# Kernel optimization log

Measured on AMD Instinct MI355X. Metric: run time of the kernel, lower is better.

## Reference

```python
import jax, jax.numpy as jnp
import numpy as np

B, S, D, H, E, K = 2, 2048, 1024, 16, 8, 2
HD = D // H          # head dim = 64 (single shared KV head: MQA)
HID = 4 * D          # MoE expert hidden dim


def _rmsnorm(x):
    # zeta SimpleRMSNorm: F.normalize(x, dim=-1) * dim**0.5
    n = jnp.linalg.norm(x, axis=-1, keepdims=True)
    return x / jnp.maximum(n, 1e-12) * (D ** 0.5)


def setup_inputs() -> dict:
    key = jax.random.key(0)
    ks = jax.random.split(key, 8)
    def w(k, shape, fan_in):
        return jax.random.normal(k, shape, jnp.float32) * (fan_in ** -0.5)
    return {
        "x":  jax.random.normal(ks[0], (B, S, D), jnp.float32),
        "Wq": w(ks[1], (D, D), D),
        "Wk": w(ks[2], (D, HD), D),
        "Wv": w(ks[3], (D, HD), D),
        "Wo": w(ks[4], (D, D), D),
        "Wg": w(ks[5], (D, E), D),
        "W1": w(ks[6], (E, D, HID), D),
        "W2": w(ks[7], (E, HID, D), HID),
    }


def reference(x, Wq, Wk, Wv, Wo, Wg, W1, W2):
    skip = x
    # --- pre-norm + multi-query attention + residual ---
    h = _rmsnorm(x)
    q = (h @ Wq).reshape(B, S, H, HD)           # [B,S,H,HD]
    k = h @ Wk                                   # [B,S,HD] shared kv head
    v = h @ Wv                                   # [B,S,HD]
    scores = jnp.einsum('bqhd,bkd->bhqk', q, k) * (HD ** -0.5)
    attn = jax.nn.softmax(scores, axis=-1)
    o = jnp.einsum('bhqk,bkd->bqhd', attn, v).reshape(B, S, D) @ Wo
    x = o + h
    # --- pre-norm + MoE (top-k softmax gating over experts) ---
    h2 = _rmsnorm(x)
    logits = h2 @ Wg                             # [B,S,E]
    topv, topi = jax.lax.top_k(logits, K)        # [B,S,K]
    gate = jax.nn.softmax(topv, axis=-1)         # renormalized top-k weights
    # dense combine weights [B,S,E], zero for unselected experts
    dense_w = jnp.sum(jax.nn.one_hot(topi, E, dtype=h2.dtype) * gate[..., None], axis=-2)
    moe_out = jnp.zeros_like(h2)
    for e in range(E):  # fixed small expert count
        ffn = jax.nn.gelu(h2 @ W1[e]) @ W2[e]
        moe_out = moe_out + dense_w[..., e:e + 1] * ffn
    return moe_out + skip
```

## Files before the change

kernel.cpp:

```cpp
#include <hip/hip_runtime.h>

typedef __bf16 bf16x8 __attribute__((ext_vector_type(8)));
typedef float f32x4 __attribute__((ext_vector_type(4)));
using u16 = unsigned short;
using u32 = unsigned int;

#define B_   2
#define S_   2048
#define D_   1024
#define E_   8
#define HID_ 4096
#define M_   4096

__device__ __forceinline__ u16 f2b_rne(float f) {
    unsigned u = __float_as_uint(f);
    u += 0x7fffu + ((u >> 16) & 1u);
    return (u16)(u >> 16);
}
__device__ __forceinline__ float b2f(u16 h) { return __uint_as_float(((unsigned)h) << 16); }
__device__ __forceinline__ void split2(float v, u16& h, u16& m) {
    h = f2b_rne(v); m = f2b_rne(v - b2f(h));
}
__device__ __forceinline__ void gld16(void* l, const void* g) {
    __builtin_amdgcn_global_load_lds((const __attribute__((address_space(1))) u32*)g,
                                     (__attribute__((address_space(3))) u32*)l, 16, 0, 0);
}

static constexpr size_t OFF_WQKVT0 = 0;
static constexpr size_t OFF_WQKVT1 = OFF_WQKVT0 + (size_t)1152*1024*2;
static constexpr size_t OFF_WOT    = OFF_WQKVT1 + (size_t)1152*1024*2;
static constexpr size_t OFF_W1T    = OFF_WOT    + (size_t)1024*1024*2;
static constexpr size_t OFF_W2T    = OFF_W1T    + (size_t)E_*HID_*D_*2;
static constexpr size_t OFF_WOWG   = OFF_W2T    + (size_t)E_*HID_*D_*2;
static constexpr size_t OFF_HF32   = OFF_WOWG   + (size_t)1024*8*4;
static constexpr size_t OFF_H0     = OFF_HF32   + (size_t)M_*D_*4;
static constexpr size_t OFF_H1     = OFF_H0     + (size_t)M_*D_*2;
static constexpr size_t OFF_H2     = OFF_H1     + (size_t)M_*D_*2;
static constexpr size_t OFF_CTL    = OFF_H2     + (size_t)M_*D_*2;
static constexpr size_t OFF_TEXP   = OFF_CTL    + 512;
static constexpr size_t OFF_TGATE  = OFF_TEXP   + (size_t)M_*2*4;
static constexpr size_t OFF_R2T    = OFF_TGATE  + (size_t)M_*2*4;
static constexpr size_t OFF_T2R    = OFF_R2T    + (size_t)9216*4;
static constexpr size_t OFF_ZROW   = OFF_T2R    + (size_t)M_*2*4;
static constexpr size_t OFF_BIG    = OFF_ZROW   + 4096;
static constexpr size_t OFF_Q0     = OFF_BIG;
static constexpr size_t OFF_Q1     = OFF_Q0   + (size_t)M_*D_*2;
static constexpr size_t OFF_KF0    = OFF_Q1   + (size_t)M_*D_*2;
static constexpr size_t OFF_KF1    = OFF_KF0  + (size_t)2*128*2*512*2;
static constexpr size_t OFF_VF0    = OFF_KF1  + (size_t)2*128*2*512*2;
static constexpr size_t OFF_VF1    = OFF_VF0  + (size_t)2*64*4*512*2;
static constexpr size_t OFF_OF32   = OFF_VF1  + (size_t)2*64*4*512*2;
static constexpr size_t OFF_AOBF   = OFF_OF32 + (size_t)M_*D_*4;
static constexpr size_t OFF_XF32   = OFF_Q0;
static constexpr size_t OFF_TACT   = OFF_BIG;
static constexpr size_t OFF_CONTR  = OFF_TACT + (size_t)9216*HID_*2;

__global__ __launch_bounds__(256) void transpose_split2_k(const float* __restrict__ in,
        u16* __restrict__ o0, u16* __restrict__ o1, int R, int C)
{
    __shared__ float tile[32][33];
    int tx = threadIdx.x & 31, ty = threadIdx.x >> 5;
    int c0 = blockIdx.x * 32, r0 = blockIdx.y * 32;
#pragma unroll
    for (int k = 0; k < 4; ++k)
        tile[ty + k*8][tx] = in[(size_t)(r0 + ty + k*8)*C + c0 + tx];
    __syncthreads();
#pragma unroll
    for (int k = 0; k < 4; ++k) {
        float v = tile[tx][ty + k*8];
        u16 h, m; split2(v, h, m);
        size_t idx = (size_t)(c0 + ty + k*8)*R + r0 + tx;
        o0[idx] = h; o1[idx] = m;
    }
}

__global__ __launch_bounds__(256) void transpose_k(const float* __restrict__ in,
                                                   u16* __restrict__ out, int R, int C)
{
    __shared__ u16 tile[32][33];
    int bz = blockIdx.z;
    in  += (size_t)bz * R * C;
    out += (size_t)bz * R * C;
    int tx = threadIdx.x & 31, ty = threadIdx.x >> 5;
    int c0 = blockIdx.x * 32, r0 = blockIdx.y * 32;
#pragma unroll
    for (int k = 0; k < 4; ++k)
        tile[ty + k*8][tx] = f2b_rne(in[(size_t)(r0 + ty + k*8)*C + c0 + tx]);
    __syncthreads();
#pragma unroll
    for (int k = 0; k < 4; ++k)
        out[(size_t)(c0 + ty + k*8)*R + r0 + tx] = tile[tx][ty + k*8];
}

__global__ __launch_bounds__(64) void wowg_k(const float* __restrict__ Wo,
                                             const float* __restrict__ Wg,
                                             float* __restrict__ wowg)
{
    int i = blockIdx.x, lane = threadIdx.x;
    const float* wr = Wo + (size_t)i*1024;
    float acc[8] = {};
#pragma unroll
    for (int j = 0; j < 16; ++j) {
        int d = j*64 + lane;
        float wv = wr[d];
        const float* g = Wg + (size_t)d*8;
        float4 g0 = *(const float4*)g, g1 = *(const float4*)(g + 4);
        acc[0] += wv*g0.x; acc[1] += wv*g0.y; acc[2] += wv*g0.z; acc[3] += wv*g0.w;
        acc[4] += wv*g1.x; acc[5] += wv*g1.y; acc[6] += wv*g1.z; acc[7] += wv*g1.w;
    }
#pragma unroll
    for (int e = 0; e < 8; ++e)
#pragma unroll
        for (int o = 32; o; o >>= 1) acc[e] += __shfl_down(acc[e], o);
    if (lane == 0) {
#pragma unroll
        for (int e = 0; e < 8; ++e) wowg[i*8 + e] = acc[e];
    }
}

__global__ __launch_bounds__(256) void rmsnorm1_k(const float* __restrict__ x,
                                                  float* __restrict__ hf,
                                                  u16* __restrict__ h0, u16* __restrict__ h1)
{
    int row = blockIdx.x, t = threadIdx.x;
    float4 v = ((const float4*)(x + (size_t)row*1024))[t];
    float ss = v.x*v.x + v.y*v.y + v.z*v.z + v.w*v.w;
#pragma unroll
    for (int o = 32; o; o >>= 1) ss += __shfl_down(ss, o);
    __shared__ float red[4];
    if ((t & 63) == 0) red[t >> 6] = ss;
    __syncthreads();
    float tot = red[0] + red[1] + red[2] + red[3];
    float sc = 32.0f / fmaxf(sqrtf(tot), 1e-12f);
    float vv[4] = {v.x*sc, v.y*sc, v.z*sc, v.w*sc};
    ((float4*)(hf + (size_t)row*1024))[t] = *(float4*)vv;
    u16 a0[4], a1[4];
#pragma unroll
    for (int j = 0; j < 4; ++j) split2(vv[j], a0[j], a1[j]);
    *(uint2*)(h0 + (size_t)row*1024 + t*4) = *(uint2*)a0;
    *(uint2*)(h1 + (size_t)row*1024 + t*4) = *(uint2*)a1;
}

__global__ __launch_bounds__(256) void gemm_qkv(
    const u16* __restrict__ A0, const u16* __restrict__ A1,
    const u16* __restrict__ B0, const u16* __restrict__ B1,
    u16* __restrict__ q0, u16* __restrict__ q1,
    u16* __restrict__ kf0, u16* __restrict__ kf1,
    u16* __restrict__ vf0, u16* __restrict__ vf1)
{
    int rb = blockIdx.x, cb = blockIdx.y;
    __shared__ __attribute__((aligned(16))) char L[24576];
    int t = threadIdx.x, w = t >> 6, lane = t & 63, r = lane & 15, g = lane >> 4;
    int wr = w >> 1, wc = w & 1;
    int arow = t >> 2, colA = (t & 3)*8;

    const char* a0c = (const char*)(A0 + (size_t)(rb*64  + arow)*1024 + colA);
    const char* a1c = (const char*)(A1 + (size_t)(rb*64  + arow)*1024 + colA);
    const char* b0c = (const char*)(B0 + (size_t)(cb*128 + arow)*1024 + colA);
    const char* b1c = (const char*)(B1 + (size_t)(cb*128 + arow)*1024 + colA);
    const size_t BH = (size_t)64*1024*2;

    int aoff[2], boff[4];
#pragma unroll
    for (int i = 0; i < 2; ++i) aoff[i] = ((wr*32 + i*16 + r)*32 + g*8)*2;
#pragma unroll
    for (int i = 0; i < 4; ++i) boff[i] = ((wc*64 + i*16 + r)*32 + g*8)*2;

    f32x4 acc[2][4] = {};
    for (int kt = 0; kt < 32; ++kt) {
        __syncthreads();
        gld16(L +          t*16, a0c + kt*64);
        gld16(L + 4096  +  t*16, a1c + kt*64);
        gld16(L + 8192  +  t*16, b0c + kt*64);
        gld16(L + 12288 +  t*16, b0c + BH + kt*64);
        gld16(L + 16384 +  t*16, b1c + kt*64);
        gld16(L + 20480 +  t*16, b1c + BH + kt*64);
        __syncthreads();
        bf16x8 a0v[2], a1v[2], b0v[4], b1v[4];
#pragma unroll
        for (int i = 0; i < 2; ++i) { a0v[i] = *(const bf16x8*)(L + aoff[i]); a1v[i] = *(const bf16x8*)(L + 4096 + aoff[i]); }
#pragma unroll
        for (int i = 0; i < 4; ++i) { b0v[i] = *(const bf16x8*)(L + 8192 + boff[i]); b1v[i] = *(const bf16x8*)(L + 16384 + boff[i]); }
#pragma unroll
        for (int mi = 0; mi < 2; ++mi)
#pragma unroll
            for (int ni = 0; ni < 4; ++ni) {
                acc[mi][ni] = __builtin_amdgcn_mfma_f32_16x16x32_bf16(a0v[mi], b0v[ni], acc[mi][ni], 0, 0, 0);
                acc[mi][ni] = __builtin_amdgcn_mfma_f32_16x16x32_bf16(a0v[mi], b1v[ni], acc[mi][ni], 0, 0, 0);
                acc[mi][ni] = __builtin_amdgcn_mfma_f32_16x16x32_bf16(a1v[mi], b0v[ni], acc[mi][ni], 0, 0, 0);
            }
    }

#pragma unroll
    for (int mi = 0; mi < 2; ++mi)
#pragma unroll
        for (int ni = 0; ni < 4; ++ni) {
            int row0 = rb*64 + wr*32 + mi*16 + g*4;
            int col  = cb*128 + wc*64 + ni*16 + r;
#pragma unroll
            for (int reg = 0; reg < 4; ++reg) {
                float val = acc[mi][ni][reg];
                int rr = row0 + reg;
                if (col < 1024) {
                    u16 hh, mm; split2(val * 0.125f, hh, mm);
                    size_t idx = (size_t)rr*1024 + col;
                    q0[idx] = hh; q1[idx] = mm;
                } else {
                    int c = col - 1024;
                    u16 hh, mm; split2(val, hh, mm);
                    int bb = rr >> 11, kv = rr & 2047;
                    if (c < 64) {
                        int ntg = kv >> 4, r2 = kv & 15, kc = c >> 5, gg = (c >> 3) & 3, j = c & 7;
                        size_t off = ((((size_t)bb*128 + ntg)*2 + kc)*64 + gg*16 + r2)*8 + j;
                        kf0[off] = hh; kf1[off] = mm;
                    } else {
                        int d = c - 64;
                        int ntg = d >> 4, r2 = d & 15, kvc = kv >> 5, gg = (kv >> 3) & 3, j = kv & 7;
                        size_t off = ((((size_t)bb*64 + kvc)*4 + ntg)*64 + gg*16 + r2)*8 + j;
                        vf0[off] = hh; vf1[off] = mm;
                    }
                }
            }
        }
}

__global__ __launch_bounds__(512) void attn_k(
    const u16* __restrict__ q0, const u16* __restrict__ q1,
    const u16* __restrict__ kfr0, const u16* __restrict__ kfr1,
    const u16* __restrict__ vfr0, const u16* __restrict__ vfr1,
    float* __restrict__ of32, u16* __restrict__ obf)
{
    int qt = blockIdx.x, h = blockIdx.y, b = blockIdx.z;
    int t = threadIdx.x, w = t >> 6, lane = t & 63, r = lane & 15, g = lane >> 4;
    __shared__ __attribute__((aligned(16))) char smem[49152];
    char* plw = smem + 32768 + w*2048;

    const char* K0c = (const char*)kfr0;
    const char* K1c = (const char*)kfr1;
    const char* V0c = (const char*)vfr0;
    const char* V1c = (const char*)vfr1;

    int qrow = b*2048 + qt*128 + w*16 + r;
    bf16x8 qf0[2], qf1[2];
#pragma unroll
    for (int kc = 0; kc < 2; ++kc) {
        size_t qi = (size_t)qrow*1024 + h*64 + kc*32 + g*8;
        qf0[kc] = *(const bf16x8*)(q0 + qi);
        qf1[kc] = *(const bf16x8*)(q1 + qi);
    }

    f32x4 accO[4] = {};
    float mrun[4], lrun[4];
#pragma unroll
    for (int reg = 0; reg < 4; ++reg) { mrun[reg] = -1e30f; lrun[reg] = 0.f; }

    for (int kt = 0; kt < 32; ++kt) {
        __syncthreads();
        {
            size_t kb = ((size_t)(b*128 + kt*4))*2048;
            size_t vb = ((size_t)(b*64  + kt*2))*4096;
            gld16(smem +          t*16, K0c + kb + t*16);
            gld16(smem + 8192  +  t*16, K1c + kb + t*16);
            gld16(smem + 16384 +  t*16, V0c + vb + t*16);
            gld16(smem + 24576 +  t*16, V1c + vb + t*16);
        }
        __syncthreads();

        f32x4 s[4] = {};
#pragma unroll
        for (int nt = 0; nt < 4; ++nt)
#pragma unroll
            for (int kc = 0; kc < 2; ++kc) {
                bf16x8 kf0 = *(const bf16x8*)(smem + (nt*2 + kc)*1024 + lane*16);
                bf16x8 kf1 = *(const bf16x8*)(smem + 8192 + (nt*2 + kc)*1024 + lane*16);
                s[nt] = __builtin_amdgcn_mfma_f32_16x16x32_bf16(qf0[kc], kf0, s[nt], 0, 0, 0);
                s[nt] = __builtin_amdgcn_mfma_f32_16x16x32_bf16(qf0[kc], kf1, s[nt], 0, 0, 0);
                s[nt] = __builtin_amdgcn_mfma_f32_16x16x32_bf16(qf1[kc], kf0, s[nt], 0, 0, 0);
            }

#pragma unroll
        for (int reg = 0; reg < 4; ++reg) {
            float mx = fmaxf(fmaxf(s[0][reg], s[1][reg]), fmaxf(s[2][reg], s[3][reg]));
#pragma unroll
            for (int d = 1; d < 16; d <<= 1) mx = fmaxf(mx, __shfl_xor(mx, d));
            float mn = fmaxf(mrun[reg], mx);
            float alpha = __expf(mrun[reg] - mn);
            float ls = 0.f;
#pragma unroll
            for (int nt = 0; nt < 4; ++nt) {
                float pv = __expf(s[nt][reg] - mn);
                s[nt][reg] = pv; ls += pv;
            }
#pragma unroll
            for (int d = 1; d < 16; d <<= 1) ls += __shfl_xor(ls, d);
            lrun[reg] = lrun[reg]*alpha + ls;
            mrun[reg] = mn;
#pragma unroll
            for (int nt = 0; nt < 4; ++nt) accO[nt][reg] *= alpha;
        }

#pragma unroll
        for (int ps = 0; ps < 2; ++ps) {
#pragma unroll
            for (int nt = 0; nt < 4; ++nt)
#pragma unroll
                for (int reg = 0; reg < 4; ++reg) {
                    float pv = s[nt][reg];
                    u16 hh = f2b_rne(pv);
                    if (ps) hh = f2b_rne(pv - b2f(hh));
                    int gr = g*4 + reg;
                    int off = (gr*128 + (nt*16 + r)*2) ^ ((gr & 7) << 4);
                    *(u16*)(plw + off) = hh;
                }
#pragma unroll
            for (int kc = 0; kc < 2; ++kc) {
                int po = (r*128 + kc*64 + g*16) ^ ((r & 7) << 4);
                bf16x8 pf = *(const bf16x8*)(plw + po);
#pragma unroll
                for (int nt = 0; nt < 4; ++nt) {
                    bf16x8 vf0 = *(const bf16x8*)(smem + 16384 + (kc*4 + nt)*1024 + lane*16);
                    accO[nt] = __builtin_amdgcn_mfma_f32_16x16x32_bf16(pf, vf0, accO[nt], 0, 0, 0);
                    if (ps == 0) {
                        bf16x8 vf1 = *(const bf16x8*)(smem + 24576 + (kc*4 + nt)*1024 + lane*16);
                        accO[nt] = __builtin_amdgcn_mfma_f32_16x16x32_bf16(pf, vf1, accO[nt], 0, 0, 0);
                    }
                }
            }
        }
    }

#pragma unroll
    for (int nt = 0; nt < 4; ++nt)
#pragma unroll
        for (int reg = 0; reg < 4; ++reg) {
            float o = accO[nt][reg] / lrun[reg];
            int row = b*2048 + qt*128 + w*16 + g*4 + reg;
            size_t idx = (size_t)row*1024 + h*64 + nt*16 + r;
            of32[idx] = o;
            obf[idx] = f2b_rne(o);
        }
}

template<int EP, bool MOE, bool INDIR>
__global__ __launch_bounds__(256) void gemm1(
    const u16* __restrict__ Abase, const u16* __restrict__ Bbase,
    u16* __restrict__ outb, float* __restrict__ outf, const float* __restrict__ addsrc,
    const int* __restrict__ r2t, const int* __restrict__ ctl, const u16* __restrict__ zrow,
    int K, int N)
{
    int rb = blockIdx.x, cb = blockIdx.y;
    if (MOE) { if (rb*128 >= ctl[16]) return; }
    const u16* Bt = Bbase;
    if (MOE) Bt += (size_t)ctl[32 + rb] * N * K;

    __shared__ __attribute__((aligned(16))) u16 As[4096];
    __shared__ __attribute__((aligned(16))) u16 Bs[4096];
    int t = threadIdx.x, w = t >> 6, lane = t & 63, r = lane & 15, g = lane >> 4;
    int wr = w >> 1, wc = w & 1;
    int arow0 = t >> 2, colA = (t & 3)*8;

    const char *gA0c, *gA1c;
    if (INDIR) {
        int tk0 = r2t[rb*128 + arow0];
        int tk1 = r2t[rb*128 + 64 + arow0];
        gA0c = (const char*)((tk0 < 0 ? zrow : Abase + (size_t)tk0*K) + colA);
        gA1c = (const char*)((tk1 < 0 ? zrow : Abase + (size_t)tk1*K) + colA);
    } else {
        gA0c = (const char*)(Abase + (size_t)(rb*128 + arow0)*K + colA);
        gA1c = (const char*)(Abase + (size_t)(rb*128 + 64 + arow0)*K + colA);
    }
    const char* gB0c = (const char*)(Bt + (size_t)(cb*128 + arow0)*K + colA);
    const char* gB1c = (const char*)(Bt + (size_t)(cb*128 + 64 + arow0)*K + colA);

    int aoff[4], boff[4];
#pragma unroll
    for (int i = 0; i < 4; ++i) {
        aoff[i] = ((wr*64 + i*16 + r)*32 + g*8)*2;
        boff[i] = ((wc*64 + i*16 + r)*32 + g*8)*2;
    }
    f32x4 acc[4][4] = {};
    int nk = K >> 5;
    for (int kt = 0; kt < nk; ++kt) {
        __syncthreads();
        gld16((char*)As + t*16,        gA0c + kt*64);
        gld16((char*)As + 4096 + t*16, gA1c + kt*64);
        gld16((char*)Bs + t*16,        gB0c + kt*64);
        gld16((char*)Bs + 4096 + t*16, gB1c + kt*64);
        __syncthreads();
        bf16x8 av[4], bv[4];
#pragma unroll
        for (int i = 0; i < 4; ++i) av[i] = *(const bf16x8*)((char*)As + aoff[i]);
#pragma unroll
        for (int i = 0; i < 4; ++i) bv[i] = *(const bf16x8*)((char*)Bs + boff[i]);
#pragma unroll
        for (int mi = 0; mi < 4; ++mi)
#pragma unroll
            for (int ni = 0; ni < 4; ++ni)
                acc[mi][ni] = __builtin_amdgcn_mfma_f32_16x16x32_bf16(av[mi], bv[ni], acc[mi][ni], 0, 0, 0);
    }

    int bm = rb*128, bn = cb*128;
#pragma unroll
    for (int mi = 0; mi < 4; ++mi)
#pragma unroll
        for (int ni = 0; ni < 4; ++ni) {
            int row0 = bm + wr*64 + mi*16 + g*4;
            int col  = bn + wc*64 + ni*16 + r;
#pragma unroll
            for (int reg = 0; reg < 4; ++reg) {
                float val = acc[mi][ni][reg];
                int rr = row0 + reg;
                size_t idx = (size_t)rr*N + col;
                if (EP == 0) {
                    outf[idx] = val + addsrc[idx];
                } else if (EP == 1) {
                    float u  = 1.5957691216f * (val + 0.044715f*val*val*val);
                    outb[idx] = f2b_rne(val / (1.0f + __expf(-u)));
                } else {
                    outb[idx] = f2b_rne(val);
                }
            }
        }
}

__global__ __launch_bounds__(256) void gemm_moe2(
    const u16* __restrict__ Abase, const u16* __restrict__ Bbase,
    u16* __restrict__ outb, const int* __restrict__ ctl)
{
    int rb = blockIdx.x, cb = blockIdx.y;
    if (rb*64 >= ctl[16]) return;
    const u16* Bt = Bbase + (size_t)ctl[32 + (rb >> 1)] * (size_t)1024 * 4096;

    __shared__ __attribute__((aligned(16))) char L[12288];
    int t = threadIdx.x, w = t >> 6, lane = t & 63, r = lane & 15, g = lane >> 4;
    int wr = w >> 1, wc = w & 1;
    int arow = t >> 2, colA = (t & 3)*8;

    const char* aC = (const char*)(Abase + (size_t)(rb*64  + arow)*4096 + colA);
    const char* bC = (const char*)(Bt    + (size_t)(cb*128 + arow)*4096 + colA);
    const size_t BH = (size_t)64*4096*2;

    int aoff[2], boff[4];
#pragma unroll
    for (int i = 0; i < 2; ++i) aoff[i] = ((wr*32 + i*16 + r)*32 + g*8)*2;
#pragma unroll
    for (int i = 0; i < 4; ++i) boff[i] = ((wc*64 + i*16 + r)*32 + g*8)*2;

    f32x4 acc[2][4] = {};
    for (int kt = 0; kt < 128; ++kt) {
        __syncthreads();
        gld16(L +         t*16, aC + kt*64);
        gld16(L + 4096 +  t*16, bC + kt*64);
        gld16(L + 8192 +  t*16, bC + BH + kt*64);
        __syncthreads();
        bf16x8 av[2], bv[4];
#pragma unroll
        for (int i = 0; i < 2; ++i) av[i] = *(const bf16x8*)(L + aoff[i]);
#pragma unroll
        for (int i = 0; i < 4; ++i) bv[i] = *(const bf16x8*)(L + 4096 + boff[i]);
#pragma unroll
        for (int mi = 0; mi < 2; ++mi)
#pragma unroll
            for (int ni = 0; ni < 4; ++ni)
                acc[mi][ni] = __builtin_amdgcn_mfma_f32_16x16x32_bf16(av[mi], bv[ni], acc[mi][ni], 0, 0, 0);
    }

#pragma unroll
    for (int mi = 0; mi < 2; ++mi)
#pragma unroll
        for (int ni = 0; ni < 4; ++ni) {
            int row0 = rb*64 + wr*32 + mi*16 + g*4;
            int col  = cb*128 + wc*64 + ni*16 + r;
#pragma unroll
            for (int reg = 0; reg < 4; ++reg)
                outb[(size_t)(row0 + reg)*1024 + col] = f2b_rne(acc[mi][ni][reg]);
        }
}

__global__ __launch_bounds__(256) void gate_k(const float* __restrict__ x2,
                                             const float* __restrict__ hrow,
                                             const float* __restrict__ orow,
                                             const float* __restrict__ Wg,
                                             const float* __restrict__ wowg,
                                             u16* __restrict__ h2,
                                             int* __restrict__ texp, float* __restrict__ tgate,
                                             int* __restrict__ ctl)
{
    int tkn = blockIdx.x*4 + (threadIdx.x >> 6);
    int lane = threadIdx.x & 63;
    const float* xr  = x2   + (size_t)tkn*1024;
    const float* hr  = hrow + (size_t)tkn*1024;
    const float* orp = orow + (size_t)tkn*1024;
    float xv[16];
    float ss = 0.f;
    float acc[8] = {};
#pragma unroll
    for (int j = 0; j < 16; ++j) {
        int d = j*64 + lane;
        float xf = xr[d]; xv[j] = xf; ss += xf*xf;
        float hf = hr[d], of = orp[d];
        const float* wg = Wg + (size_t)d*8;
        const float* wo = wowg + (size_t)d*8;
        float4 a0 = *(const float4*)wg, a1 = *(const float4*)(wg + 4);
        float4 b0 = *(const float4*)wo, b1 = *(const float4*)(wo + 4);
        acc[0] += hf*a0.x + of*b0.x; acc[1] += hf*a0.y + of*b0.y;
        acc[2] += hf*a0.z + of*b0.z; acc[3] += hf*a0.w + of*b0.w;
        acc[4] += hf*a1.x + of*b1.x; acc[5] += hf*a1.y + of*b1.y;
        acc[6] += hf*a1.z + of*b1.z; acc[7] += hf*a1.w + of*b1.w;
    }
#pragma unroll
    for (int o = 32; o; o >>= 1) ss += __shfl_down(ss, o);
    ss = __shfl(ss, 0);
    float sc = 32.0f / fmaxf(sqrtf(ss), 1e-12f);
#pragma unroll
    for (int j = 0; j < 16; ++j)
        h2[(size_t)tkn*1024 + j*64 + lane] = f2b_rne(xv[j]*sc);
#pragma unroll
    for (int e = 0; e < 8; ++e)
#pragma unroll
        for (int o = 32; o; o >>= 1) acc[e] += __shfl_down(acc[e], o);
    if (lane == 0) {
        float lg[8];
#pragma unroll
        for (int e = 0; e < 8; ++e) lg[e] = acc[e]*sc;
        int i0 = 0; float v0 = lg[0];
#pragma unroll
        for (int e = 1; e < 8; ++e) if (lg[e] > v0) { v0 = lg[e]; i0 = e; }
        int i1 = -1; float v1 = -1e30f;
#pragma unroll
        for (int e = 0; e < 8; ++e) if (e != i0 && lg[e] > v1) { v1 = lg[e]; i1 = e; }
        float g0 = 1.0f / (1.0f + __expf(v1 - v0));
        texp[tkn*2] = i0; texp[tkn*2+1] = i1;
        tgate[tkn*2] = g0; tgate[tkn*2+1] = 1.0f - g0;
        atomicAdd(&ctl[i0], 1); atomicAdd(&ctl[i1], 1);
    }
}

__global__ void plan_k(int* ctl, int* r2t)
{
    if (threadIdx.x == 0) {
        int off = 0;
        for (int e = 0; e < 8; ++e) {
            int c = ctl[e];
            ctl[8 + e] = off;
            int p = (c + 127) & ~127;
            int rb0 = off >> 7, nrbe = p >> 7;
            for (int i = 0; i < nrbe; ++i) ctl[32 + rb0 + i] = e;
            off += p;
        }
        ctl[16] = off; ctl[17] = off >> 7;
    }
    __syncthreads();
    for (int i = threadIdx.x; i < 9216; i += blockDim.x) r2t[i] = -1;
}

__global__ __launch_bounds__(256) void assign_k(const int* __restrict__ texp, int* ctl,
                                                int* __restrict__ r2t, int* __restrict__ t2r)
{
    int tkn = blockIdx.x*256 + threadIdx.x;
    if (tkn >= M_) return;
#pragma unroll
    for (int kk = 0; kk < 2; ++kk) {
        int e = texp[tkn*2 + kk];
        int pos = atomicAdd(&ctl[8 + e], 1);
        r2t[pos] = tkn;
        t2r[tkn*2 + kk] = pos;
    }
}

__global__ __launch_bounds__(256) void combine_k(const float* __restrict__ xin,
                                                 const u16* __restrict__ contrib,
                                                 const int* __restrict__ t2r,
                                                 const float* __restrict__ tgate,
                                                 float* __restrict__ out)
{
    int tkn = blockIdx.x;
    int c = threadIdx.x*4;
    int r0 = t2r[tkn*2], r1 = t2r[tkn*2+1];
    float g0 = tgate[tkn*2], g1 = tgate[tkn*2+1];
    float4 sk = *(const float4*)(xin + (size_t)tkn*1024 + c);
    const u16* c0p = contrib + (size_t)r0*1024 + c;
    const u16* c1p = contrib + (size_t)r1*1024 + c;
    float4 o;
    o.x = sk.x + g0*b2f(c0p[0]) + g1*b2f(c1p[0]);
    o.y = sk.y + g0*b2f(c0p[1]) + g1*b2f(c1p[1]);
    o.z = sk.z + g0*b2f(c0p[2]) + g1*b2f(c1p[2]);
    o.w = sk.w + g0*b2f(c0p[3]) + g1*b2f(c1p[3]);
    *(float4*)(out + (size_t)tkn*1024 + c) = o;
}

extern "C" void kernel_launch(void* const* d_in, const int* in_sizes, int n_in,
                              void* d_out, int out_size, void* d_ws, size_t ws_size,
                              hipStream_t stream)
{
    const float* x  = (const float*)d_in[0];
    const float* Wq = (const float*)d_in[1];
    const float* Wk = (const float*)d_in[2];
    const float* Wv = (const float*)d_in[3];
    const float* Wo = (const float*)d_in[4];
    const float* Wg = (const float*)d_in[5];
    const float* W1 = (const float*)d_in[6];
    const float* W2 = (const float*)d_in[7];
    float* out = (float*)d_out;

    char* ws = (char*)d_ws;
    auto U = [&](size_t off) { return (u16*)(ws + off); };
    auto F = [&](size_t off) { return (float*)(ws + off); };
    int*   CTL  = (int*)(ws + OFF_CTL);
    int*   TEXP = (int*)(ws + OFF_TEXP);
    float* TGATE= (float*)(ws + OFF_TGATE);
    int*   R2T  = (int*)(ws + OFF_R2T);
    int*   T2R  = (int*)(ws + OFF_T2R);

    hipMemsetAsync(ws + OFF_CTL,  0, 512,  stream);
    hipMemsetAsync(ws + OFF_ZROW, 0, 4096, stream);

    dim3 tb(256);
    transpose_split2_k<<<dim3(32, 32), tb, 0, stream>>>(Wq, U(OFF_WQKVT0), U(OFF_WQKVT1), 1024, 1024);
    transpose_split2_k<<<dim3(2, 32),  tb, 0, stream>>>(Wk, U(OFF_WQKVT0) + (size_t)1024*1024, U(OFF_WQKVT1) + (size_t)1024*1024, 1024, 64);
    transpose_split2_k<<<dim3(2, 32),  tb, 0, stream>>>(Wv, U(OFF_WQKVT0) + (size_t)1088*1024, U(OFF_WQKVT1) + (size_t)1088*1024, 1024, 64);
    transpose_k<<<dim3(32, 32, 1), tb, 0, stream>>>(Wo, U(OFF_WOT), 1024, 1024);
    transpose_k<<<dim3(128, 32, 8), tb, 0, stream>>>(W1, U(OFF_W1T), 1024, 4096);
    transpose_k<<<dim3(32, 128, 8), tb, 0, stream>>>(W2, U(OFF_W2T), 4096, 1024);
    wowg_k<<<1024, 64, 0, stream>>>(Wo, Wg, F(OFF_WOWG));

    rmsnorm1_k<<<M_, 256, 0, stream>>>(x, F(OFF_HF32), U(OFF_H0), U(OFF_H1));

    gemm_qkv<<<dim3(64, 9), tb, 0, stream>>>(U(OFF_H0), U(OFF_H1),
        U(OFF_WQKVT0), U(OFF_WQKVT1),
        U(OFF_Q0), U(OFF_Q1), U(OFF_KF0), U(OFF_KF1), U(OFF_VF0), U(OFF_VF1));

    attn_k<<<dim3(16, 16, 2), dim3(512), 0, stream>>>(U(OFF_Q0), U(OFF_Q1),
        U(OFF_KF0), U(OFF_KF1), U(OFF_VF0), U(OFF_VF1), F(OFF_OF32), U(OFF_AOBF));

    gemm1<0, false, false><<<dim3(32, 8), tb, 0, stream>>>(U(OFF_AOBF), U(OFF_WOT),
        nullptr, F(OFF_XF32), F(OFF_HF32), nullptr, nullptr, nullptr, 1024, 1024);

    gate_k<<<1024, 256, 0, stream>>>(F(OFF_XF32), F(OFF_HF32), F(OFF_OF32), Wg, F(OFF_WOWG),
        U(OFF_H2), TEXP, TGATE, CTL);
    plan_k<<<1, 256, 0, stream>>>(CTL, R2T);
    assign_k<<<16, 256, 0, stream>>>(TEXP, CTL, R2T, T2R);

    gemm1<1, true, true ><<<dim3(72, 32), tb, 0, stream>>>(U(OFF_H2), U(OFF_W1T),
        U(OFF_TACT), nullptr, nullptr, R2T, CTL, U(OFF_ZROW), 1024, 4096);
    gemm_moe2<<<dim3(144, 8), tb, 0, stream>>>(U(OFF_TACT), U(OFF_W2T), U(OFF_CONTR), CTL);

    combine_k<<<M_, 256, 0, stream>>>(x, U(OFF_CONTR), T2R, TGATE, out);
}
```

Baseline: 1.080 ms.

## Vectorize weight transposes, stage GEMM epilogues through LDS, shrink attention blocks

```diff
diff --git a/kernel.cpp b/kernel.cpp
--- a/kernel.cpp
+++ b/kernel.cpp
@@ -92,6 +92,35 @@
         out[(size_t)(c0 + ty + k*8)*R + r0 + tx] = tile[tx][ty + k*8];
 }
 
+__global__ __launch_bounds__(256) void transpose_v_k(const float* __restrict__ in,
+                                                     u16* __restrict__ out, int R, int C)
+{
+    __shared__ u16 tile[64][72];
+    int bz = blockIdx.z;
+    in  += (size_t)bz * R * C;
+    out += (size_t)bz * R * C;
+    int c0 = blockIdx.x * 64, r0 = blockIdx.y * 64;
+    int tr = threadIdx.x >> 4, tc4 = (threadIdx.x & 15) * 4;
+#pragma unroll
+    for (int p = 0; p < 4; ++p) {
+        float4 v = *(const float4*)(in + (size_t)(r0 + tr + p*16)*C + c0 + tc4);
+        tile[tr + p*16][tc4 + 0] = f2b_rne(v.x);
+        tile[tr + p*16][tc4 + 1] = f2b_rne(v.y);
+        tile[tr + p*16][tc4 + 2] = f2b_rne(v.z);
+        tile[tr + p*16][tc4 + 3] = f2b_rne(v.w);
+    }
+    __syncthreads();
+    int orw = threadIdx.x >> 3, occ = (threadIdx.x & 7) * 8;
+#pragma unroll
+    for (int q = 0; q < 2; ++q) {
+        int orow = orw + q*32;
+        u16 vals[8];
+#pragma unroll
+        for (int j = 0; j < 8; ++j) vals[j] = tile[occ + j][orow];
+        *(uint4*)(out + (size_t)(c0 + orow)*R + r0 + occ) = *(uint4*)vals;
+    }
+}
+
 __global__ __launch_bounds__(64) void wowg_k(const float* __restrict__ Wo,
                                              const float* __restrict__ Wg,
                                              float* __restrict__ wowg)
@@ -224,7 +253,7 @@
         }
 }
 
-__global__ __launch_bounds__(512) void attn_k(
+__global__ __launch_bounds__(256) void attn_k(
     const u16* __restrict__ q0, const u16* __restrict__ q1,
     const u16* __restrict__ kfr0, const u16* __restrict__ kfr1,
     const u16* __restrict__ vfr0, const u16* __restrict__ vfr1,
@@ -232,7 +261,7 @@
 {
     int qt = blockIdx.x, h = blockIdx.y, b = blockIdx.z;
     int t = threadIdx.x, w = t >> 6, lane = t & 63, r = lane & 15, g = lane >> 4;
-    __shared__ __attribute__((aligned(16))) char smem[49152];
+    __shared__ __attribute__((aligned(16))) char smem[40960];
     char* plw = smem + 32768 + w*2048;
 
     const char* K0c = (const char*)kfr0;
@@ -240,7 +269,7 @@
     const char* V0c = (const char*)vfr0;
     const char* V1c = (const char*)vfr1;
 
-    int qrow = b*2048 + qt*128 + w*16 + r;
+    int qrow = b*2048 + qt*64 + w*16 + r;
     bf16x8 qf0[2], qf1[2];
 #pragma unroll
     for (int kc = 0; kc < 2; ++kc) {
@@ -258,11 +287,15 @@
         __syncthreads();
         {
             size_t kb = ((size_t)(b*128 + kt*4))*2048;
-            size_t vb = ((size_t)(b*64  + kt*2))*4096;
-            gld16(smem +          t*16, K0c + kb + t*16);
-            gld16(smem + 8192  +  t*16, K1c + kb + t*16);
-            gld16(smem + 16384 +  t*16, V0c + vb + t*16);
-            gld16(smem + 24576 +  t*16, V1c + vb + t*16);
+            gld16(smem +         t*16, K0c + kb + t*16);
+            gld16(smem + 4096  + t*16, K0c + kb + 4096 + t*16);
+            gld16(smem + 8192  + t*16, K1c + kb + t*16);
+            gld16(smem + 12288 + t*16, K1c + kb + 4096 + t*16);
+            size_t vb = ((size_t)(b*64 + kt*2))*4096;
+            gld16(smem + 16384 + t*16, V0c + vb + t*16);
+            gld16(smem + 20480 + t*16, V0c + vb + 4096 + t*16);
+            gld16(smem + 24576 + t*16, V1c + vb + t*16);
+            gld16(smem + 28672 + t*16, V1c + vb + 4096 + t*16);
         }
         __syncthreads();
 
@@ -334,7 +367,7 @@
 #pragma unroll
         for (int reg = 0; reg < 4; ++reg) {
             float o = accO[nt][reg] / lrun[reg];
-            int row = b*2048 + qt*128 + w*16 + g*4 + reg;
+            int row = b*2048 + qt*64 + w*16 + g*4 + reg;
             size_t idx = (size_t)row*1024 + h*64 + nt*16 + r;
             of32[idx] = o;
             obf[idx] = f2b_rne(o);
@@ -353,8 +386,9 @@
     const u16* Bt = Bbase;
     if (MOE) Bt += (size_t)ctl[32 + rb] * N * K;
 
-    __shared__ __attribute__((aligned(16))) u16 As[4096];
-    __shared__ __attribute__((aligned(16))) u16 Bs[4096];
+    __shared__ __attribute__((aligned(16))) u16 SM[8192];
+    char* As = (char*)SM;
+    char* Bs = (char*)SM + 8192;
     int t = threadIdx.x, w = t >> 6, lane = t & 63, r = lane & 15, g = lane >> 4;
     int wr = w >> 1, wc = w & 1;
     int arow0 = t >> 2, colA = (t & 3)*8;
@@ -382,16 +416,16 @@
     int nk = K >> 5;
     for (int kt = 0; kt < nk; ++kt) {
         __syncthreads();
-        gld16((char*)As + t*16,        gA0c + kt*64);
-        gld16((char*)As + 4096 + t*16, gA1c + kt*64);
-        gld16((char*)Bs + t*16,        gB0c + kt*64);
-        gld16((char*)Bs + 4096 + t*16, gB1c + kt*64);
+        gld16(As + t*16,        gA0c + kt*64);
+        gld16(As + 4096 + t*16, gA1c + kt*64);
+        gld16(Bs + t*16,        gB0c + kt*64);
+        gld16(Bs + 4096 + t*16, gB1c + kt*64);
         __syncthreads();
         bf16x8 av[4], bv[4];
 #pragma unroll
-        for (int i = 0; i < 4; ++i) av[i] = *(const bf16x8*)((char*)As + aoff[i]);
-#pragma unroll
-        for (int i = 0; i < 4; ++i) bv[i] = *(const bf16x8*)((char*)Bs + boff[i]);
+        for (int i = 0; i < 4; ++i) av[i] = *(const bf16x8*)(As + aoff[i]);
+#pragma unroll
+        for (int i = 0; i < 4; ++i) bv[i] = *(const bf16x8*)(Bs + boff[i]);
 #pragma unroll
         for (int mi = 0; mi < 4; ++mi)
 #pragma unroll
@@ -400,27 +434,42 @@
     }
 
     int bm = rb*128, bn = cb*128;
-#pragma unroll
-    for (int mi = 0; mi < 4; ++mi)
-#pragma unroll
-        for (int ni = 0; ni < 4; ++ni) {
-            int row0 = bm + wr*64 + mi*16 + g*4;
-            int col  = bn + wc*64 + ni*16 + r;
-#pragma unroll
-            for (int reg = 0; reg < 4; ++reg) {
-                float val = acc[mi][ni][reg];
-                int rr = row0 + reg;
-                size_t idx = (size_t)rr*N + col;
-                if (EP == 0) {
+    if (EP == 1) {
+        __syncthreads();
+        u16* eb = SM + w*1152;
+#pragma unroll
+        for (int mi = 0; mi < 4; ++mi) {
+#pragma unroll
+            for (int ni = 0; ni < 4; ++ni)
+#pragma unroll
+                for (int reg = 0; reg < 4; ++reg) {
+                    float val = acc[mi][ni][reg];
+                    float u  = 1.5957691216f * (val + 0.044715f*val*val*val);
+                    eb[(g*4 + reg)*72 + ni*16 + r] = f2b_rne(val / (1.0f + __expf(-u)));
+                }
+#pragma unroll
+            for (int q = 0; q < 2; ++q) {
+                int idx = q*64 + lane;
+                int row = idx >> 3, colc = (idx & 7)*8;
+                uint4 vv = *(const uint4*)(eb + row*72 + colc);
+                *(uint4*)(outb + (size_t)(bm + wr*64 + mi*16 + row)*N + bn + wc*64 + colc) = vv;
+            }
+        }
+    } else {
+#pragma unroll
+        for (int mi = 0; mi < 4; ++mi)
+#pragma unroll
+            for (int ni = 0; ni < 4; ++ni) {
+                int row0 = bm + wr*64 + mi*16 + g*4;
+                int col  = bn + wc*64 + ni*16 + r;
+#pragma unroll
+                for (int reg = 0; reg < 4; ++reg) {
+                    float val = acc[mi][ni][reg];
+                    size_t idx = (size_t)(row0 + reg)*N + col;
                     outf[idx] = val + addsrc[idx];
-                } else if (EP == 1) {
-                    float u  = 1.5957691216f * (val + 0.044715f*val*val*val);
-                    outb[idx] = f2b_rne(val / (1.0f + __expf(-u)));
-                } else {
-                    outb[idx] = f2b_rne(val);
                 }
             }
-        }
+    }
 }
 
 __global__ __launch_bounds__(256) void gemm_moe2(
@@ -465,16 +514,23 @@
                 acc[mi][ni] = __builtin_amdgcn_mfma_f32_16x16x32_bf16(av[mi], bv[ni], acc[mi][ni], 0, 0, 0);
     }
 
-#pragma unroll
-    for (int mi = 0; mi < 2; ++mi)
-#pragma unroll
-        for (int ni = 0; ni < 4; ++ni) {
-            int row0 = rb*64 + wr*32 + mi*16 + g*4;
-            int col  = cb*128 + wc*64 + ni*16 + r;
+    __syncthreads();
+    u16* eb = (u16*)L + w*1152;
+#pragma unroll
+    for (int mi = 0; mi < 2; ++mi) {
+#pragma unroll
+        for (int ni = 0; ni < 4; ++ni)
 #pragma unroll
             for (int reg = 0; reg < 4; ++reg)
-                outb[(size_t)(row0 + reg)*1024 + col] = f2b_rne(acc[mi][ni][reg]);
+                eb[(g*4 + reg)*72 + ni*16 + r] = f2b_rne(acc[mi][ni][reg]);
+#pragma unroll
+        for (int q = 0; q < 2; ++q) {
+            int idx = q*64 + lane;
+            int row = idx >> 3, colc = (idx & 7)*8;
+            uint4 vv = *(const uint4*)(eb + row*72 + colc);
+            *(uint4*)(outb + (size_t)(rb*64 + wr*32 + mi*16 + row)*1024 + cb*128 + wc*64 + colc) = vv;
         }
+    }
 }
 
 __global__ __launch_bounds__(256) void gate_k(const float* __restrict__ x2,
@@ -620,8 +676,8 @@
     transpose_split2_k<<<dim3(2, 32),  tb, 0, stream>>>(Wk, U(OFF_WQKVT0) + (size_t)1024*1024, U(OFF_WQKVT1) + (size_t)1024*1024, 1024, 64);
     transpose_split2_k<<<dim3(2, 32),  tb, 0, stream>>>(Wv, U(OFF_WQKVT0) + (size_t)1088*1024, U(OFF_WQKVT1) + (size_t)1088*1024, 1024, 64);
     transpose_k<<<dim3(32, 32, 1), tb, 0, stream>>>(Wo, U(OFF_WOT), 1024, 1024);
-    transpose_k<<<dim3(128, 32, 8), tb, 0, stream>>>(W1, U(OFF_W1T), 1024, 4096);
-    transpose_k<<<dim3(32, 128, 8), tb, 0, stream>>>(W2, U(OFF_W2T), 4096, 1024);
+    transpose_v_k<<<dim3(64, 16, 8), tb, 0, stream>>>(W1, U(OFF_W1T), 1024, 4096);
+    transpose_v_k<<<dim3(16, 64, 8), tb, 0, stream>>>(W2, U(OFF_W2T), 4096, 1024);
     wowg_k<<<1024, 64, 0, stream>>>(Wo, Wg, F(OFF_WOWG));
 
     rmsnorm1_k<<<M_, 256, 0, stream>>>(x, F(OFF_HF32), U(OFF_H0), U(OFF_H1));
@@ -630,7 +686,7 @@
         U(OFF_WQKVT0), U(OFF_WQKVT1),
         U(OFF_Q0), U(OFF_Q1), U(OFF_KF0), U(OFF_KF1), U(OFF_VF0), U(OFF_VF1));
 
-    attn_k<<<dim3(16, 16, 2), dim3(512), 0, stream>>>(U(OFF_Q0), U(OFF_Q1),
+    attn_k<<<dim3(32, 16, 2), tb, 0, stream>>>(U(OFF_Q0), U(OFF_Q1),
         U(OFF_KF0), U(OFF_KF1), U(OFF_VF0), U(OFF_VF1), F(OFF_OF32), U(OFF_AOBF));
 
     gemm1<0, false, false><<<dim3(32, 8), tb, 0, stream>>>(U(OFF_AOBF), U(OFF_WOT),
```

New measurement: 1.056 ms. 1.02x faster.
